# Kernel optimization log

Measured on AMD Instinct MI355X. Metric: run time of the kernel, lower is better.

The kernel has to match this reference:

```python
import jax, jax.numpy as jnp
import numpy as np

H = 150  # hidden per direction

def _lstm_dir(x, w_ih, w_hh, b_ih, b_hh):
    # x: [B, T, D] -> hs: [B, T, H]; PyTorch gate order i,f,g,o
    B = x.shape[0]
    xg = jnp.einsum('btd,gd->btg', x, w_ih) + b_ih + b_hh  # precompute input projection [B,T,4H]
    def step(carry, xt):
        h, c = carry
        g = xt + h @ w_hh.T
        i, f, gg, o = jnp.split(g, 4, axis=-1)
        i, f, o = jax.nn.sigmoid(i), jax.nn.sigmoid(f), jax.nn.sigmoid(o)
        c = f * c + i * jnp.tanh(gg)
        h = o * jnp.tanh(c)
        return (h, c), h
    init = (jnp.zeros((B, H), x.dtype), jnp.zeros((B, H), x.dtype))
    _, hs = jax.lax.scan(step, init, jnp.swapaxes(xg, 0, 1))  # [T,B,H]
    return jnp.swapaxes(hs, 0, 1)

def _bilstm(x, w_ih_f, w_hh_f, b_ih_f, b_hh_f, w_ih_b, w_hh_b, b_ih_b, b_hh_b):
    fwd = _lstm_dir(x, w_ih_f, w_hh_f, b_ih_f, b_hh_f)
    bwd = jnp.flip(_lstm_dir(jnp.flip(x, axis=1), w_ih_b, w_hh_b, b_ih_b, b_hh_b), axis=1)
    return jnp.concatenate([fwd, bwd], axis=-1)  # [B, T, 2H]

def setup_inputs() -> dict:
    key = jax.random.key(0)
    ks = jax.random.split(key, 20)
    s = 0.05
    d = {
        'sentences': jax.random.normal(ks[0], (1024, 128, 343), jnp.float32),
        'w_ih_f1': jax.random.normal(ks[1], (600, 343)) * s,
        'w_hh_f1': jax.random.normal(ks[2], (600, 150)) * s,
        'b_ih_f1': jax.random.normal(ks[3], (600,)) * s,
        'b_hh_f1': jax.random.normal(ks[4], (600,)) * s,
        'w_ih_b1': jax.random.normal(ks[5], (600, 343)) * s,
        'w_hh_b1': jax.random.normal(ks[6], (600, 150)) * s,
        'b_ih_b1': jax.random.normal(ks[7], (600,)) * s,
        'b_hh_b1': jax.random.normal(ks[8], (600,)) * s,
        'w_ih_f2': jax.random.normal(ks[9], (600, 300)) * s,
        'w_hh_f2': jax.random.normal(ks[10], (600, 150)) * s,
        'b_ih_f2': jax.random.normal(ks[11], (600,)) * s,
        'b_hh_f2': jax.random.normal(ks[12], (600,)) * s,
        'w_ih_b2': jax.random.normal(ks[13], (600, 300)) * s,
        'w_hh_b2': jax.random.normal(ks[14], (600, 150)) * s,
        'b_ih_b2': jax.random.normal(ks[15], (600,)) * s,
        'b_hh_b2': jax.random.normal(ks[16], (600,)) * s,
        'w_out': jax.random.normal(ks[17], (7, 300)) * s,
        'b_out': jax.random.normal(ks[18], (7,)) * s,
    }
    return d

def reference(sentences, w_ih_f1, w_hh_f1, b_ih_f1, b_hh_f1, w_ih_b1, w_hh_b1, b_ih_b1, b_hh_b1,
              w_ih_f2, w_hh_f2, b_ih_f2, b_hh_f2, w_ih_b2, w_hh_b2, b_ih_b2, b_hh_b2, w_out, b_out):
    # Layer 1: per-sentence BiLSTM over words, batched instead of a python loop (dropout is eval-mode identity)
    word_out = _bilstm(sentences, w_ih_f1, w_hh_f1, b_ih_f1, b_hh_f1, w_ih_b1, w_hh_b1, b_ih_b1, b_hh_b1)  # [S,T,300]
    sent_emb = jnp.max(word_out, axis=1)  # max-pool over words -> [S,300]
    # Layer 2: BiLSTM over the sequence of sentence embeddings (batch of 1 paragraph)
    sent_out = _bilstm(sent_emb[None], w_ih_f2, w_hh_f2, b_ih_f2, b_hh_f2, w_ih_b2, w_hh_b2, b_ih_b2, b_hh_b2)[0]  # [S,300]
    log_probs = jax.nn.log_softmax(sent_out @ w_out.T + b_out, axis=-1)  # [S,7]
    return log_probs
```

## Files before the change

### kernel.cpp

```cpp
#include <hip/hip_runtime.h>
#include <hip/hip_bf16.h>
#include <hip/hip_fp16.h>

typedef short bf16x8 __attribute__((ext_vector_type(8)));
typedef float f32x4 __attribute__((ext_vector_type(4)));
typedef unsigned short u16x4 __attribute__((ext_vector_type(4)));
typedef unsigned int uint32;

#define MFMA_B16(a,b,c) __builtin_amdgcn_mfma_f32_16x16x32_bf16(a,b,c,0,0,0)

#define NS   1024
#define TLEN 128
#define DD   343
#define HH   150
#define GG   600
#define KX   352
#define XR   360
#define HR   168
#define KXP  44
#define NP   640
#define NG2  640

#define OFF_WXP  0u
#define OFF_WHP  901120u
#define OFF_B1   1310720u
#define OFF_W2B  1315840u
#define OFF_W2I  1725440u
#define OFF_SE   3184640u
#define OFF_XG2  4413440u
#define OFF_H2O  9656320u
#define OFF_XBF  10885120u
#define NEED_BF  103159808ull
#define OFF_XG1  103159808ull
#define NEED_SPLIT 774248448ull

#define PE0 450560
#define PE1 655360
#define PE2 656640
#define PE3 861440
#define PE4 1226240

__device__ __forceinline__ float rcp_fast(float x) { return __builtin_amdgcn_rcpf(x); }
__device__ __forceinline__ float sigm(float x) { return rcp_fast(1.f + __expf(-x)); }
__device__ __forceinline__ float tanh_fast(float x) { return 1.f - 2.f * rcp_fast(__expf(2.f * x) + 1.f); }

typedef __attribute__((address_space(1))) const void GASV;
typedef __attribute__((address_space(3))) void LASV;
__device__ __forceinline__ void gload_lds16(const void* g, void* l) {
  __builtin_amdgcn_global_load_lds((GASV*)g, (LASV*)l, 16, 0, 0);
}

__device__ __forceinline__ void bar_lds() {
  asm volatile("s_waitcnt lgkmcnt(0)" ::: "memory");
  __builtin_amdgcn_s_barrier();
  asm volatile("" ::: "memory");
}
__device__ __forceinline__ void bar_full() {
  asm volatile("s_waitcnt vmcnt(0) lgkmcnt(0)" ::: "memory");
  __builtin_amdgcn_s_barrier();
  asm volatile("" ::: "memory");
}

__device__ __forceinline__ unsigned short f2bu(float v) {
  __hip_bfloat16 b = __float2bfloat16(v);
  return __builtin_bit_cast(unsigned short, b);
}

__global__ __launch_bounds__(256) void prep_kernel(
    const float* __restrict__ wif1, const float* __restrict__ whf1,
    const float* __restrict__ bif1, const float* __restrict__ bhf1,
    const float* __restrict__ wib1, const float* __restrict__ whb1,
    const float* __restrict__ bib1, const float* __restrict__ bhb1,
    const float* __restrict__ wif2, const float* __restrict__ wib2,
    const float* __restrict__ whf2, const float* __restrict__ whb2,
    __hip_bfloat16* __restrict__ WXp, __hip_bfloat16* __restrict__ WHp,
    float* __restrict__ B1, __hip_bfloat16* __restrict__ W2B, float* __restrict__ W2I)
{
  int i = blockIdx.x * 256 + threadIdx.x;
  if (i < PE0) {
    int d = i / 225280; int r = i - d * 225280;
    int p = r / 5120;   int r2 = r - p * 5120;
    int n2 = r2 >> 3;   int jj = r2 & 7;
    int k = p * 8 + jj;
    int g = n2 / 160, j = n2 - g * 160;
    const float* w = d ? wib1 : wif1;
    float v = (j < HH && k < DD) ? w[(g * HH + j) * DD + k] : 0.f;
    WXp[i] = __float2bfloat16(v);
  } else if (i < PE1) {
    int ii = i - PE0;
    int d = ii / 102400; int r = ii - d * 102400;
    int p = r / 5120;    int r2 = r - p * 5120;
    int n2 = r2 >> 3;    int jj = r2 & 7;
    int k = p * 8 + jj;
    int g = n2 / 160, j = n2 - g * 160;
    const float* w = d ? whb1 : whf1;
    float v = (j < HH && k < HH) ? w[(g * HH + j) * HH + k] : 0.f;
    WHp[ii] = __float2bfloat16(v);
  } else if (i < PE2) {
    int ii = i - PE1;
    int d = ii / NP; int n2 = ii - d * NP;
    int g = n2 / 160, j = n2 - g * 160;
    float v = 0.f;
    if (j < HH) {
      int n = g * HH + j;
      v = d ? (bib1[n] + bhb1[n]) : (bif1[n] + bhf1[n]);
    }
    B1[ii] = v;
  } else if (i < PE3) {
    int ii = i - PE2;
    int d = ii / 102400; int r = ii - d * 102400;
    int n2 = r / 160;    int k = r - n2 * 160;
    int g = n2 / 160, j = n2 - g * 160;
    const float* w = d ? whb2 : whf2;
    float v = (j < HH && k < HH) ? w[(g * HH + j) * HH + k] : 0.f;
    W2B[ii] = __float2bfloat16(v);
  } else if (i < PE4) {
    int ii = i - PE3;
    int d = ii / 182400; int r = ii - d * 182400;
    int k = r / 608;     int n = r - k * 608;
    const float* w = d ? wib2 : wif2;
    float v = (n < GG) ? w[n * 300 + k] : 0.f;
    W2I[ii] = v;
  }
}

__global__ __launch_bounds__(256) void xcvt_kernel(
    const float* __restrict__ x, __hip_bfloat16* __restrict__ XBF)
{
  const int total4 = NS * TLEN * (KX / 4);
  for (int idx = blockIdx.x * 256 + threadIdx.x; idx < total4; idx += gridDim.x * 256) {
    int row = idx / 88;
    int c4 = (idx - row * 88) * 4;
    const float* src = x + (size_t)row * DD + c4;
    float v0 = 0.f, v1 = 0.f, v2 = 0.f, v3 = 0.f;
    if (c4 + 3 < DD) {
      v0 = __builtin_nontemporal_load(src);
      v1 = __builtin_nontemporal_load(src + 1);
      v2 = __builtin_nontemporal_load(src + 2);
      v3 = __builtin_nontemporal_load(src + 3);
    } else {
      if (c4 < DD)     v0 = src[0];
      if (c4 + 1 < DD) v1 = src[1];
      if (c4 + 2 < DD) v2 = src[2];
    }
    u16x4 o;
    o.x = f2bu(v0); o.y = f2bu(v1); o.z = f2bu(v2); o.w = f2bu(v3);
    u16x4* dst = (u16x4*)((unsigned short*)XBF + (size_t)row * KX + c4);
    __builtin_nontemporal_store(o, dst);
  }
}

#define GA_SMEM (128u * 720u)

__global__ __launch_bounds__(512) void xg1_gemm(
    const __hip_bfloat16* __restrict__ XBF, const __hip_bfloat16* __restrict__ WXp,
    const float* __restrict__ B1, float* __restrict__ XG1)
{
  extern __shared__ char smem[];
  __hip_bfloat16* xsA = (__hip_bfloat16*)smem;

  const int bid = blockIdx.x;
  const int mt = bid / 10;
  const int ntile = bid - mt * 10;
  const int dir = ntile / 5;
  const int nb = (ntile - dir * 5) * 128;
  const int m0 = mt * 128;

  const int tid = threadIdx.x;
  const int lane = tid & 63;
  const int wv = tid >> 6;
  const int wr = wv >> 2;
  const int wc = wv & 3;
  const int arow = lane & 15;
  const int kgrp = lane >> 4;

  #pragma unroll
  for (int i = 0; i < 16; ++i) {
    int rid = wv * 16 + i;
    if (lane < 44) {
      const __hip_bfloat16* gp = XBF + (size_t)(m0 + rid) * KX + lane * 8;
      gload_lds16((const void*)gp, (void*)(smem + rid * 720));
    }
  }
  bar_full();

  const __hip_bfloat16* WXd = WXp + (size_t)dir * KXP * NP * 8;

  f32x4 acc[4][2];
  #pragma unroll
  for (int mi = 0; mi < 4; ++mi)
    #pragma unroll
    for (int ni = 0; ni < 2; ++ni) acc[mi][ni] = (f32x4){0.f, 0.f, 0.f, 0.f};

  for (int kk = 0; kk < 11; ++kk) {
    bf16x8 a[4], b[2];
    #pragma unroll
    for (int mi = 0; mi < 4; ++mi)
      a[mi] = *reinterpret_cast<const bf16x8*>(
          xsA + (wr * 64 + mi * 16 + arow) * XR + kk * 32 + kgrp * 8);
    #pragma unroll
    for (int ni = 0; ni < 2; ++ni)
      b[ni] = *reinterpret_cast<const bf16x8*>(
          WXd + ((size_t)(kk * 4 + kgrp) * NP + nb + wc * 32 + ni * 16 + arow) * 8);
    #pragma unroll
    for (int mi = 0; mi < 4; ++mi)
      #pragma unroll
      for (int ni = 0; ni < 2; ++ni)
        acc[mi][ni] = MFMA_B16(a[mi], b[ni], acc[mi][ni]);
  }

  float bias[2];
  #pragma unroll
  for (int ni = 0; ni < 2; ++ni)
    bias[ni] = B1[dir * NP + nb + wc * 32 + ni * 16 + arow];

  float* outd = XG1 + (size_t)dir * NS * TLEN * NG2;
  #pragma unroll
  for (int mi = 0; mi < 4; ++mi) {
    #pragma unroll
    for (int r = 0; r < 4; ++r) {
      int m = m0 + wr * 64 + mi * 16 + kgrp * 4 + r;
      int s = m >> 7, t = m & 127;
      float* row = outd + ((size_t)s * TLEN + t) * NG2;
      #pragma unroll
      for (int ni = 0; ni < 2; ++ni)
        row[nb + wc * 32 + ni * 16 + arow] = acc[mi][ni][r] + bias[ni];
    }
  }
}

__global__ __launch_bounds__(640) void lstm1_rec(
    const float* __restrict__ XG1, const __hip_bfloat16* __restrict__ WHp,
    float* __restrict__ SE)
{
  __shared__ __hip_bfloat16 hs[16 * HR];

  const int tid = threadIdx.x;
  const int lane = tid & 63;
  const int wv = tid >> 6;
  const int dir = blockIdx.x & 1;
  const int s0 = (blockIdx.x >> 1) * 8;
  const int c16 = lane & 15;
  const int kgrp = lane >> 4;
  const int j = wv * 16 + c16;

  for (int e = tid; e < 16 * HR; e += 640) hs[e] = __float2bfloat16(0.f);

  const __hip_bfloat16* WHd = WHp + (size_t)dir * 20 * NP * 8;
  bf16x8 whr[5][4];
  #pragma unroll
  for (int kh = 0; kh < 5; ++kh)
    #pragma unroll
    for (int g4 = 0; g4 < 4; ++g4) {
      whr[kh][g4] = *reinterpret_cast<const bf16x8*>(
          WHd + ((size_t)(kh * 4 + kgrp) * NP + g4 * 160 + j) * 8);
      asm volatile("" : "+v"(whr[kh][g4]));
    }

  float creg[4] = {0.f, 0.f, 0.f, 0.f};
  float mxr[4] = {-3e38f, -3e38f, -3e38f, -3e38f};

  const float* xgd = XG1 + (size_t)dir * NS * TLEN * NG2;
  const int sentb = s0 + (kgrp & 1) * 4;
  const int par = kgrp >> 1;

  float xq[16], xqN[16];
  #pragma unroll
  for (int g4 = 0; g4 < 4; ++g4)
    #pragma unroll
    for (int r = 0; r < 4; ++r) {
      int tl = par;
      int tt = dir ? (127 - tl) : tl;
      xq[g4 * 4 + r] = xgd[((size_t)(sentb + r) * TLEN + tt) * NG2 + g4 * 160 + j];
    }
  __syncthreads();

  for (int p = 0; p < 64; ++p) {
    f32x4 acc[4];
    #pragma unroll
    for (int g4 = 0; g4 < 4; ++g4) {
      acc[g4][0] = xq[g4 * 4 + 0]; acc[g4][1] = xq[g4 * 4 + 1];
      acc[g4][2] = xq[g4 * 4 + 2]; acc[g4][3] = xq[g4 * 4 + 3];
    }
    if (p < 63) {
      #pragma unroll
      for (int g4 = 0; g4 < 4; ++g4)
        #pragma unroll
        for (int r = 0; r < 4; ++r) {
          int tl = 2 * (p + 1) + par;
          int tt = dir ? (127 - tl) : tl;
          xqN[g4 * 4 + r] = xgd[((size_t)(sentb + r) * TLEN + tt) * NG2 + g4 * 160 + j];
        }
    }
    #pragma unroll
    for (int kh = 0; kh < 5; ++kh) {
      bf16x8 ah = *reinterpret_cast<const bf16x8*>(hs + c16 * HR + kh * 32 + kgrp * 8);
      #pragma unroll
      for (int g4 = 0; g4 < 4; ++g4)
        acc[g4] = MFMA_B16(ah, whr[kh][g4], acc[g4]);
    }
    {
      const bool act = (kgrp < 2);
      #pragma unroll
      for (int r = 0; r < 4; ++r) {
        float iv = sigm(acc[0][r]);
        float fv = sigm(acc[1][r]);
        float gv = tanh_fast(acc[2][r]);
        float ov = sigm(acc[3][r]);
        float cin = __shfl_xor(creg[r], 32);
        float cn = fv * cin + iv * gv;
        float h = ov * tanh_fast(cn);
        creg[r] = act ? cn : creg[r];
        mxr[r] = act ? fmaxf(mxr[r], h) : mxr[r];
        if (act) hs[(8 + kgrp * 4 + r) * HR + j] = __float2bfloat16(h);
      }
    }
    bar_lds();
    #pragma unroll
    for (int kh = 0; kh < 5; ++kh) {
      bf16x8 ah = *reinterpret_cast<const bf16x8*>(hs + c16 * HR + kh * 32 + kgrp * 8);
      #pragma unroll
      for (int g4 = 0; g4 < 4; ++g4)
        acc[g4] = MFMA_B16(ah, whr[kh][g4], acc[g4]);
    }
    {
      const bool act = (kgrp >= 2);
      #pragma unroll
      for (int r = 0; r < 4; ++r) {
        float iv = sigm(acc[0][r]);
        float fv = sigm(acc[1][r]);
        float gv = tanh_fast(acc[2][r]);
        float ov = sigm(acc[3][r]);
        float cin = __shfl_xor(creg[r], 32);
        float cn = fv * cin + iv * gv;
        float h = ov * tanh_fast(cn);
        creg[r] = act ? cn : creg[r];
        mxr[r] = act ? fmaxf(mxr[r], h) : mxr[r];
        if (act) {
          int s = (kgrp - 2) * 4 + r;
          hs[s * HR + j] = __float2bfloat16(h);
          hs[(8 + s) * HR + j] = __float2bfloat16(0.f);
        }
      }
    }
    bar_lds();
    #pragma unroll
    for (int q = 0; q < 16; ++q) xq[q] = xqN[q];
  }

  #pragma unroll
  for (int r = 0; r < 4; ++r) {
    float m = fmaxf(mxr[r], __shfl_xor(mxr[r], 32));
    if (kgrp < 2 && j < HH)
      SE[(size_t)(s0 + kgrp * 4 + r) * 300 + dir * HH + j] = m;
  }
}

#define XS_SZ   46080u
#define HS_OFF  (2u * XS_SZ)
#define L1_SMEM (HS_OFF + 5376u)

template<bool BF>
__device__ __forceinline__ void stage_x(char* xsd, const float* __restrict__ x,
                                        const __hip_bfloat16* __restrict__ XBF,
                                        int t0, int dir, int s0, int tid, int lane, int wv)
{
  if constexpr (BF) {
    #pragma unroll
    for (int i = 0; i < 7; ++i) {
      int rid = wv + i * 10;
      if (rid < 64 && lane < 44) {
        int p = rid >> 4, rr = rid & 15;
        int t = t0 + 2 * p + (rr >> 3);
        int s = s0 + (rr & 7);
        int tt = dir ? (127 - t) : t;
        const __hip_bfloat16* gp = XBF + ((size_t)s * TLEN + tt) * KX + lane * 8;
        gload_lds16((const void*)gp, (void*)(xsd + rid * 720));
      }
    }
  } else {
    for (int e = tid; e < 4 * 16 * XR; e += 640) {
      int row16 = e / XR;
      int col = e - row16 * XR;
      int p = row16 >> 4, rr = row16 & 15;
      int t = t0 + 2 * p + (rr >> 3);
      int s = s0 + (rr & 7);
      int tt = dir ? (127 - t) : t;
      float v = (col < DD) ? x[((size_t)s * TLEN + tt) * DD + col] : 0.f;
      ((__hip_bfloat16*)xsd)[e] = __float2bfloat16(v);
    }
  }
}

template<bool BF>
__global__ __launch_bounds__(640)
void lstm1_kernel(
    const float* __restrict__ x, const __hip_bfloat16* __restrict__ XBF,
    const __hip_bfloat16* __restrict__ WXp, const __hip_bfloat16* __restrict__ WHp,
    const float* __restrict__ B1, float* __restrict__ SE)
{
  extern __shared__ char smem[];
  char* xs0 = smem;
  char* xs1 = smem + XS_SZ;
  __hip_bfloat16* hs = (__hip_bfloat16*)(smem + HS_OFF);

  const int tid = threadIdx.x;
  const int lane = tid & 63;
  const int wv = tid >> 6;
  const int dir = blockIdx.x & 1;
  const int s0 = (blockIdx.x >> 1) * 8;
  const int c16 = lane & 15;
  const int kgrp = lane >> 4;
  const int j = wv * 16 + c16;

  for (int e = tid; e < 16 * HR; e += 640) hs[e] = __float2bfloat16(0.f);

  float bias[4];
  #pragma unroll
  for (int g4 = 0; g4 < 4; ++g4) {
    bias[g4] = B1[dir * NP + g4 * 160 + j];
    asm volatile("" : "+v"(bias[g4]));
  }

  const __hip_bfloat16* WXd = WXp + (size_t)dir * KXP * NP * 8;
  const __hip_bfloat16* WHd = WHp + (size_t)dir * 20 * NP * 8;

  bf16x8 whr[5][4];
  #pragma unroll
  for (int kh = 0; kh < 5; ++kh)
    #pragma unroll
    for (int g4 = 0; g4 < 4; ++g4) {
      whr[kh][g4] = *reinterpret_cast<const bf16x8*>(
          WHd + ((size_t)(kh * 4 + kgrp) * NP + g4 * 160 + j) * 8);
      asm volatile("" : "+v"(whr[kh][g4]));
    }

  float creg[4] = {0.f, 0.f, 0.f, 0.f};
  float mxr[4] = {-3e38f, -3e38f, -3e38f, -3e38f};

  stage_x<BF>(xs0, x, XBF, 0, dir, s0, tid, lane, wv);
  bar_full();

  for (int g = 0; g < 16; ++g) {
    char* xsc = (g & 1) ? xs1 : xs0;
    char* xsn = (g & 1) ? xs0 : xs1;
    const __hip_bfloat16* xsb = (const __hip_bfloat16*)xsc;

    f32x4 acc[4][4];
    #pragma unroll
    for (int p = 0; p < 4; ++p)
      #pragma unroll
      for (int g4 = 0; g4 < 4; ++g4) acc[p][g4] = (f32x4){0.f, 0.f, 0.f, 0.f};

    for (int kk = 0; kk < 11; ++kk) {
      bf16x8 a[4], b[4];
      #pragma unroll
      for (int p = 0; p < 4; ++p)
        a[p] = *reinterpret_cast<const bf16x8*>(xsb + (p * 16 + c16) * XR + kk * 32 + kgrp * 8);
      #pragma unroll
      for (int g4 = 0; g4 < 4; ++g4)
        b[g4] = *reinterpret_cast<const bf16x8*>(
            WXd + ((size_t)(kk * 4 + kgrp) * NP + g4 * 160 + j) * 8);
      #pragma unroll
      for (int p = 0; p < 4; ++p)
        #pragma unroll
        for (int g4 = 0; g4 < 4; ++g4)
          acc[p][g4] = MFMA_B16(a[p], b[g4], acc[p][g4]);
    }

    if (g < 15)
      stage_x<BF>(xsn, x, XBF, (g + 1) * 8, dir, s0, tid, lane, wv);

    #pragma unroll
    for (int p = 0; p < 4; ++p) {
      #pragma unroll
      for (int kh = 0; kh < 5; ++kh) {
        bf16x8 ah = *reinterpret_cast<const bf16x8*>(hs + c16 * HR + kh * 32 + kgrp * 8);
        #pragma unroll
        for (int g4 = 0; g4 < 4; ++g4)
          acc[p][g4] = MFMA_B16(ah, whr[kh][g4], acc[p][g4]);
      }
      {
        const bool act = (kgrp < 2);
        #pragma unroll
        for (int r = 0; r < 4; ++r) {
          float iv = sigm(acc[p][0][r] + bias[0]);
          float fv = sigm(acc[p][1][r] + bias[1]);
          float gv = tanh_fast(acc[p][2][r] + bias[2]);
          float ov = sigm(acc[p][3][r] + bias[3]);
          float cin = __shfl_xor(creg[r], 32);
          float cn = fv * cin + iv * gv;
          float h = ov * tanh_fast(cn);
          creg[r] = act ? cn : creg[r];
          mxr[r] = act ? fmaxf(mxr[r], h) : mxr[r];
          if (act) hs[(8 + kgrp * 4 + r) * HR + j] = __float2bfloat16(h);
        }
      }
      bar_lds();
      #pragma unroll
      for (int kh = 0; kh < 5; ++kh) {
        bf16x8 ah = *reinterpret_cast<const bf16x8*>(hs + c16 * HR + kh * 32 + kgrp * 8);
        #pragma unroll
        for (int g4 = 0; g4 < 4; ++g4)
          acc[p][g4] = MFMA_B16(ah, whr[kh][g4], acc[p][g4]);
      }
      {
        const bool act = (kgrp >= 2);
        #pragma unroll
        for (int r = 0; r < 4; ++r) {
          float iv = sigm(acc[p][0][r] + bias[0]);
          float fv = sigm(acc[p][1][r] + bias[1]);
          float gv = tanh_fast(acc[p][2][r] + bias[2]);
          float ov = sigm(acc[p][3][r] + bias[3]);
          float cin = __shfl_xor(creg[r], 32);
          float cn = fv * cin + iv * gv;
          float h = ov * tanh_fast(cn);
          creg[r] = act ? cn : creg[r];
          mxr[r] = act ? fmaxf(mxr[r], h) : mxr[r];
          if (act) {
            int s = (kgrp - 2) * 4 + r;
            hs[s * HR + j] = __float2bfloat16(h);
            hs[(8 + s) * HR + j] = __float2bfloat16(0.f);
          }
        }
      }
      if (p == 3) bar_full(); else bar_lds();
    }
  }

  #pragma unroll
  for (int r = 0; r < 4; ++r) {
    float m = fmaxf(mxr[r], __shfl_xor(mxr[r], 32));
    if (kgrp < 2 && j < HH)
      SE[(size_t)(s0 + kgrp * 4 + r) * 300 + dir * HH + j] = m;
  }
}

__global__ __launch_bounds__(256, 1) void xg2_kernel(
    const float* __restrict__ SE, const float* __restrict__ W2I,
    const float* __restrict__ bif2, const float* __restrict__ bhf2,
    const float* __restrict__ bib2, const float* __restrict__ bhb2,
    float* __restrict__ XG2)
{
  __shared__ float se[32 * 304];
  const int d = blockIdx.x >> 5, st = blockIdx.x & 31, sb = st * 32;
  const int tid = threadIdx.x;
  for (int e = tid; e < 32 * 300; e += 256) {
    int si = e / 300, k = e - si * 300;
    se[si * 304 + k] = SE[(size_t)(sb + si) * 300 + k];
  }
  __syncthreads();
  for (int pass = 0; pass < 3; ++pass) {
    int n = pass * 256 + tid;
    if (n < GG) {
      int n2 = (n / 150) * 160 + (n % 150);
      float bias = d ? (bib2[n] + bhb2[n]) : (bif2[n] + bhf2[n]);
      float acc[32];
      #pragma unroll
      for (int si = 0; si < 32; ++si) acc[si] = bias;
      const float* wcol = W2I + (size_t)d * 300 * 608 + n;
      for (int k = 0; k < 300; ++k) {
        float wvv = wcol[(size_t)k * 608];
        #pragma unroll
        for (int si = 0; si < 32; ++si) acc[si] += wvv * se[si * 304 + k];
      }
      #pragma unroll
      for (int si = 0; si < 32; ++si)
        XG2[((size_t)d * NS + sb + si) * NG2 + n2] = acc[si];
    }
  }
  for (int e = tid; e < 32 * 40; e += 256) {
    int si = e / 40, q = e - si * 40;
    int g = q / 10, jp = 150 + (q - g * 10);
    XG2[((size_t)d * NS + sb + si) * NG2 + g * 160 + jp] = 0.f;
  }
}

__global__ __launch_bounds__(640) void lstm2_kernel(
    const __hip_bfloat16* __restrict__ W2B, const float* __restrict__ XG2,
    float* __restrict__ H2O)
{
  const int dir = blockIdx.x;
  const int tid = threadIdx.x;
  const int lane = tid & 63;
  const int wv = tid >> 6;
  const int c16 = lane & 15;
  const int kg = lane >> 4;
  const int j = wv * 16 + c16;
  __shared__ __align__(16) __hip_bfloat16 hbuf[2][160];

  const f32x4 ZERO4 = {0.f, 0.f, 0.f, 0.f};

  const __hip_bfloat16* Wd = W2B + (size_t)dir * NP * 160;
  bf16x8 wf[5][4];
  #pragma unroll
  for (int kt = 0; kt < 5; ++kt)
    #pragma unroll
    for (int g4 = 0; g4 < 4; ++g4) {
      wf[kt][g4] = *reinterpret_cast<const bf16x8*>(
          Wd + (size_t)(g4 * 160 + j) * 160 + kt * 32 + kg * 8);
      asm volatile("" : "+v"(wf[kt][g4]));
    }

  if (tid < 160) hbuf[0][tid] = __float2bfloat16(0.f);
  __syncthreads();

  float creg = 0.f;
  const float* xg = XG2 + (size_t)dir * NS * NG2;

  float xqC[8], xqN[8];
  #pragma unroll
  for (int q = 0; q < 2; ++q)
    #pragma unroll
    for (int g4 = 0; g4 < 4; ++g4) {
      int sl = q;
      int ss2 = dir ? (1023 - sl) : sl;
      xqC[q * 4 + g4] = xg[(size_t)ss2 * NG2 + g4 * 160 + j];
    }

  for (int grp = 0; grp < 512; ++grp) {
    #pragma unroll
    for (int q = 0; q < 2; ++q)
      #pragma unroll
      for (int g4 = 0; g4 < 4; ++g4) {
        int sl = grp * 2 + 2 + q;
        if (sl < 1024) {
          int ss2 = dir ? (1023 - sl) : sl;
          xqN[q * 4 + g4] = xg[(size_t)ss2 * NG2 + g4 * 160 + j];
        } else {
          xqN[q * 4 + g4] = 0.f;
        }
      }
    #pragma unroll
    for (int q = 0; q < 2; ++q) {
      const int step = grp * 2 + q;
      const int ss = dir ? (1023 - step) : step;
      bf16x8 hf[5];
      #pragma unroll
      for (int kt = 0; kt < 5; ++kt)
        hf[kt] = *reinterpret_cast<const bf16x8*>(&hbuf[q][kt * 32 + kg * 8]);
      f32x4 aA[4], aB[4];
      #pragma unroll
      for (int g4 = 0; g4 < 4; ++g4) {
        aA[g4] = MFMA_B16(hf[0], wf[0][g4], ZERO4);
        aB[g4] = MFMA_B16(hf[1], wf[1][g4], ZERO4);
      }
      #pragma unroll
      for (int g4 = 0; g4 < 4; ++g4) {
        aA[g4] = MFMA_B16(hf[2], wf[2][g4], aA[g4]);
        aB[g4] = MFMA_B16(hf[3], wf[3][g4], aB[g4]);
        aA[g4] = MFMA_B16(hf[4], wf[4][g4], aA[g4]);
      }
      float iv = sigm(aA[0][0] + aB[0][0] + xqC[q * 4 + 0]);
      float fv = sigm(aA[1][0] + aB[1][0] + xqC[q * 4 + 1]);
      float gv = tanh_fast(aA[2][0] + aB[2][0] + xqC[q * 4 + 2]);
      float ov = sigm(aA[3][0] + aB[3][0] + xqC[q * 4 + 3]);
      creg = fv * creg + iv * gv;
      float nh = ov * tanh_fast(creg);
      if (kg == 0) {
        hbuf[q ^ 1][j] = __float2bfloat16(nh);
        if (j < HH) H2O[(size_t)ss * 300 + dir * HH + j] = nh;
      }
      bar_lds();
    }
    #pragma unroll
    for (int q = 0; q < 8; ++q) xqC[q] = xqN[q];
  }
}

__global__ __launch_bounds__(256, 1) void head_kernel(
    const float* __restrict__ H2O, const float* __restrict__ w_out,
    const float* __restrict__ b_out, float* __restrict__ out)
{
  int s = blockIdx.x * 256 + threadIdx.x;
  if (s >= NS) return;
  float acc[7];
  #pragma unroll
  for (int c = 0; c < 7; ++c) acc[c] = b_out[c];
  const float* hrow = H2O + (size_t)s * 300;
  for (int k = 0; k < 300; ++k) {
    float hv = hrow[k];
    #pragma unroll
    for (int c = 0; c < 7; ++c) acc[c] += hv * w_out[c * 300 + k];
  }
  float m = acc[0];
  #pragma unroll
  for (int c = 1; c < 7; ++c) m = fmaxf(m, acc[c]);
  float sum = 0.f;
  #pragma unroll
  for (int c = 0; c < 7; ++c) sum += __expf(acc[c] - m);
  float lse = m + __logf(sum);
  #pragma unroll
  for (int c = 0; c < 7; ++c) out[s * 7 + c] = acc[c] - lse;
}

extern "C" void kernel_launch(void* const* d_in, const int* in_sizes, int n_in,
                              void* d_out, int out_size, void* d_ws, size_t ws_size,
                              hipStream_t stream) {
  const float* x      = (const float*)d_in[0];
  const float* wif1   = (const float*)d_in[1];
  const float* whf1   = (const float*)d_in[2];
  const float* bif1   = (const float*)d_in[3];
  const float* bhf1   = (const float*)d_in[4];
  const float* wib1   = (const float*)d_in[5];
  const float* whb1   = (const float*)d_in[6];
  const float* bib1   = (const float*)d_in[7];
  const float* bhb1   = (const float*)d_in[8];
  const float* wif2   = (const float*)d_in[9];
  const float* whf2   = (const float*)d_in[10];
  const float* bif2   = (const float*)d_in[11];
  const float* bhf2   = (const float*)d_in[12];
  const float* wib2   = (const float*)d_in[13];
  const float* whb2   = (const float*)d_in[14];
  const float* bib2   = (const float*)d_in[15];
  const float* bhb2   = (const float*)d_in[16];
  const float* w_out  = (const float*)d_in[17];
  const float* b_out  = (const float*)d_in[18];

  char* ws = (char*)d_ws;
  __hip_bfloat16* WXp = (__hip_bfloat16*)(ws + OFF_WXP);
  __hip_bfloat16* WHp = (__hip_bfloat16*)(ws + OFF_WHP);
  float*    B1  = (float*)(ws + OFF_B1);
  __hip_bfloat16* W2B = (__hip_bfloat16*)(ws + OFF_W2B);
  float*    W2I = (float*)(ws + OFF_W2I);
  float*    SE  = (float*)(ws + OFF_SE);
  float*    XG2 = (float*)(ws + OFF_XG2);
  float*    H2O = (float*)(ws + OFF_H2O);
  __hip_bfloat16* XBF = (__hip_bfloat16*)(ws + OFF_XBF);
  float*    XG1 = (float*)(ws + OFF_XG1);

  const bool useBF = (ws_size >= NEED_BF);
  const bool useSPLIT = (ws_size >= NEED_SPLIT);

  prep_kernel<<<(PE4 + 255) / 256, 256, 0, stream>>>(
      wif1, whf1, bif1, bhf1, wib1, whb1, bib1, bhb1,
      wif2, wib2, whf2, whb2, WXp, WHp, B1, W2B, W2I);

  if (useBF)
    xcvt_kernel<<<4096, 256, 0, stream>>>(x, XBF);

  if (useSPLIT) {
    (void)hipFuncSetAttribute((const void*)xg1_gemm,
                              hipFuncAttributeMaxDynamicSharedMemorySize, GA_SMEM);
    xg1_gemm<<<10240, 512, GA_SMEM, stream>>>(XBF, WXp, B1, XG1);
    lstm1_rec<<<256, 640, 0, stream>>>(XG1, WHp, SE);
  } else {
    (void)hipFuncSetAttribute((const void*)(lstm1_kernel<true>),
                              hipFuncAttributeMaxDynamicSharedMemorySize, L1_SMEM);
    (void)hipFuncSetAttribute((const void*)(lstm1_kernel<false>),
                              hipFuncAttributeMaxDynamicSharedMemorySize, L1_SMEM);
    if (useBF)
      lstm1_kernel<true><<<256, 640, L1_SMEM, stream>>>(x, XBF, WXp, WHp, B1, SE);
    else
      lstm1_kernel<false><<<256, 640, L1_SMEM, stream>>>(x, XBF, WXp, WHp, B1, SE);
  }

  xg2_kernel<<<64, 256, 0, stream>>>(SE, W2I, bif2, bhf2, bib2, bhb2, XG2);

  lstm2_kernel<<<2, 640, 0, stream>>>(W2B, XG2, H2O);

  head_kernel<<<4, 256, 0, stream>>>(H2O, w_out, b_out, (float*)d_out);
}
```

Before: 1.610 ms.

## Store layer-1 input projections as bf16 and process sentences in chunks

```diff
diff --git a/kernel.cpp b/kernel.cpp
--- a/kernel.cpp
+++ b/kernel.cpp
@@ -32,7 +32,6 @@
 #define OFF_XBF  10885120u
 #define NEED_BF  103159808ull
 #define OFF_XG1  103159808ull
-#define NEED_SPLIT 774248448ull
 
 #define PE0 450560
 #define PE1 655360
@@ -154,84 +153,85 @@
 
 __global__ __launch_bounds__(512) void xg1_gemm(
     const __hip_bfloat16* __restrict__ XBF, const __hip_bfloat16* __restrict__ WXp,
-    const float* __restrict__ B1, float* __restrict__ XG1)
+    const float* __restrict__ B1, __hip_bfloat16* __restrict__ XG1,
+    int sBase, int CS)
 {
   extern __shared__ char smem[];
   __hip_bfloat16* xsA = (__hip_bfloat16*)smem;
 
   const int bid = blockIdx.x;
-  const int mt = bid / 10;
-  const int ntile = bid - mt * 10;
-  const int dir = ntile / 5;
-  const int nb = (ntile - dir * 5) * 128;
-  const int m0 = mt * 128;
+  const int dir = bid & 1;
+  const int mtl = bid >> 1;
+  const int sg = sBase + mtl;
 
   const int tid = threadIdx.x;
   const int lane = tid & 63;
   const int wv = tid >> 6;
   const int wr = wv >> 2;
   const int wc = wv & 3;
-  const int arow = lane & 15;
+  const int c16 = lane & 15;
   const int kgrp = lane >> 4;
 
   #pragma unroll
   for (int i = 0; i < 16; ++i) {
     int rid = wv * 16 + i;
     if (lane < 44) {
-      const __hip_bfloat16* gp = XBF + (size_t)(m0 + rid) * KX + lane * 8;
+      const __hip_bfloat16* gp = XBF + ((size_t)sg * TLEN + rid) * KX + lane * 8;
       gload_lds16((const void*)gp, (void*)(smem + rid * 720));
     }
   }
   bar_full();
 
   const __hip_bfloat16* WXd = WXp + (size_t)dir * KXP * NP * 8;
-
-  f32x4 acc[4][2];
-  #pragma unroll
-  for (int mi = 0; mi < 4; ++mi)
-    #pragma unroll
-    for (int ni = 0; ni < 2; ++ni) acc[mi][ni] = (f32x4){0.f, 0.f, 0.f, 0.f};
-
-  for (int kk = 0; kk < 11; ++kk) {
-    bf16x8 a[4], b[2];
+  __hip_bfloat16* outd = XG1 + ((size_t)dir * CS + mtl) * TLEN * NG2;
+
+  #pragma unroll
+  for (int nh = 0; nh < 2; ++nh) {
+    const int nbase = nh * 320 + wc * 80;
+    f32x4 acc[4][5];
     #pragma unroll
     for (int mi = 0; mi < 4; ++mi)
-      a[mi] = *reinterpret_cast<const bf16x8*>(
-          xsA + (wr * 64 + mi * 16 + arow) * XR + kk * 32 + kgrp * 8);
-    #pragma unroll
-    for (int ni = 0; ni < 2; ++ni)
-      b[ni] = *reinterpret_cast<const bf16x8*>(
-          WXd + ((size_t)(kk * 4 + kgrp) * NP + nb + wc * 32 + ni * 16 + arow) * 8);
+      #pragma unroll
+      for (int nf = 0; nf < 5; ++nf) acc[mi][nf] = (f32x4){0.f, 0.f, 0.f, 0.f};
+
+    for (int kk = 0; kk < 11; ++kk) {
+      bf16x8 a[4], b[5];
+      #pragma unroll
+      for (int mi = 0; mi < 4; ++mi)
+        a[mi] = *reinterpret_cast<const bf16x8*>(
+            xsA + (wr * 64 + mi * 16 + c16) * XR + kk * 32 + kgrp * 8);
+      #pragma unroll
+      for (int nf = 0; nf < 5; ++nf)
+        b[nf] = *reinterpret_cast<const bf16x8*>(
+            WXd + ((size_t)(kk * 4 + kgrp) * NP + nbase + nf * 16 + c16) * 8);
+      #pragma unroll
+      for (int mi = 0; mi < 4; ++mi)
+        #pragma unroll
+        for (int nf = 0; nf < 5; ++nf)
+          acc[mi][nf] = MFMA_B16(a[mi], b[nf], acc[mi][nf]);
+    }
+
+    float bias[5];
+    #pragma unroll
+    for (int nf = 0; nf < 5; ++nf)
+      bias[nf] = B1[dir * NP + nbase + nf * 16 + c16];
+
     #pragma unroll
     for (int mi = 0; mi < 4; ++mi)
       #pragma unroll
-      for (int ni = 0; ni < 2; ++ni)
-        acc[mi][ni] = MFMA_B16(a[mi], b[ni], acc[mi][ni]);
-  }
-
-  float bias[2];
-  #pragma unroll
-  for (int ni = 0; ni < 2; ++ni)
-    bias[ni] = B1[dir * NP + nb + wc * 32 + ni * 16 + arow];
-
-  float* outd = XG1 + (size_t)dir * NS * TLEN * NG2;
-  #pragma unroll
-  for (int mi = 0; mi < 4; ++mi) {
-    #pragma unroll
-    for (int r = 0; r < 4; ++r) {
-      int m = m0 + wr * 64 + mi * 16 + kgrp * 4 + r;
-      int s = m >> 7, t = m & 127;
-      float* row = outd + ((size_t)s * TLEN + t) * NG2;
-      #pragma unroll
-      for (int ni = 0; ni < 2; ++ni)
-        row[nb + wc * 32 + ni * 16 + arow] = acc[mi][ni][r] + bias[ni];
-    }
+      for (int r = 0; r < 4; ++r) {
+        int t = wr * 64 + mi * 16 + kgrp * 4 + r;
+        __hip_bfloat16* row = outd + (size_t)t * NG2;
+        #pragma unroll
+        for (int nf = 0; nf < 5; ++nf)
+          row[nbase + nf * 16 + c16] = __float2bfloat16(acc[mi][nf][r] + bias[nf]);
+      }
   }
 }
 
 __global__ __launch_bounds__(640) void lstm1_rec(
-    const float* __restrict__ XG1, const __hip_bfloat16* __restrict__ WHp,
-    float* __restrict__ SE)
+    const __hip_bfloat16* __restrict__ XG1, const __hip_bfloat16* __restrict__ WHp,
+    float* __restrict__ SE, int sBase, int CS)
 {
   __shared__ __hip_bfloat16 hs[16 * HR];
 
@@ -239,7 +239,9 @@
   const int lane = tid & 63;
   const int wv = tid >> 6;
   const int dir = blockIdx.x & 1;
-  const int s0 = (blockIdx.x >> 1) * 8;
+  const int grp = blockIdx.x >> 1;
+  const int cls0 = grp * 8;
+  const int s0g = sBase + cls0;
   const int c16 = lane & 15;
   const int kgrp = lane >> 4;
   const int j = wv * 16 + c16;
@@ -260,8 +262,8 @@
   float creg[4] = {0.f, 0.f, 0.f, 0.f};
   float mxr[4] = {-3e38f, -3e38f, -3e38f, -3e38f};
 
-  const float* xgd = XG1 + (size_t)dir * NS * TLEN * NG2;
-  const int sentb = s0 + (kgrp & 1) * 4;
+  const __hip_bfloat16* xgd = XG1 + (size_t)dir * CS * TLEN * NG2;
+  const int sentb = cls0 + (kgrp & 1) * 4;
   const int par = kgrp >> 1;
 
   float xq[16], xqN[16];
@@ -269,9 +271,9 @@
   for (int g4 = 0; g4 < 4; ++g4)
     #pragma unroll
     for (int r = 0; r < 4; ++r) {
-      int tl = par;
-      int tt = dir ? (127 - tl) : tl;
-      xq[g4 * 4 + r] = xgd[((size_t)(sentb + r) * TLEN + tt) * NG2 + g4 * 160 + j];
+      int tt = dir ? (127 - par) : par;
+      xq[g4 * 4 + r] = __bfloat162float(
+          xgd[((size_t)(sentb + r) * TLEN + tt) * NG2 + g4 * 160 + j]);
     }
   __syncthreads();
 
@@ -289,7 +291,8 @@
         for (int r = 0; r < 4; ++r) {
           int tl = 2 * (p + 1) + par;
           int tt = dir ? (127 - tl) : tl;
-          xqN[g4 * 4 + r] = xgd[((size_t)(sentb + r) * TLEN + tt) * NG2 + g4 * 160 + j];
+          xqN[g4 * 4 + r] = __bfloat162float(
+              xgd[((size_t)(sentb + r) * TLEN + tt) * NG2 + g4 * 160 + j]);
         }
     }
     #pragma unroll
@@ -352,7 +355,7 @@
   for (int r = 0; r < 4; ++r) {
     float m = fmaxf(mxr[r], __shfl_xor(mxr[r], 32));
     if (kgrp < 2 && j < HH)
-      SE[(size_t)(s0 + kgrp * 4 + r) * 300 + dir * HH + j] = m;
+      SE[(size_t)(s0g + kgrp * 4 + r) * 300 + dir * HH + j] = m;
   }
 }
 
@@ -613,8 +616,7 @@
   for (int q = 0; q < 2; ++q)
     #pragma unroll
     for (int g4 = 0; g4 < 4; ++g4) {
-      int sl = q;
-      int ss2 = dir ? (1023 - sl) : sl;
+      int ss2 = dir ? (1023 - q) : q;
       xqC[q * 4 + g4] = xg[(size_t)ss2 * NG2 + g4 * 160 + j];
     }
 
@@ -727,10 +729,16 @@
   float*    XG2 = (float*)(ws + OFF_XG2);
   float*    H2O = (float*)(ws + OFF_H2O);
   __hip_bfloat16* XBF = (__hip_bfloat16*)(ws + OFF_XBF);
-  float*    XG1 = (float*)(ws + OFF_XG1);
+  __hip_bfloat16* XG1 = (__hip_bfloat16*)(ws + OFF_XG1);
 
   const bool useBF = (ws_size >= NEED_BF);
-  const bool useSPLIT = (ws_size >= NEED_SPLIT);
+
+  int CS = 0;
+  if (useBF && ws_size >= NEED_BF + 128ull * 327680ull) {
+    size_t avail = ws_size - NEED_BF;
+    CS = 1024;
+    while ((size_t)CS * 327680ull > avail) CS >>= 1;
+  }
 
   prep_kernel<<<(PE4 + 255) / 256, 256, 0, stream>>>(
       wif1, whf1, bif1, bhf1, wib1, whb1, bib1, bhb1,
@@ -739,11 +747,13 @@
   if (useBF)
     xcvt_kernel<<<4096, 256, 0, stream>>>(x, XBF);
 
-  if (useSPLIT) {
+  if (CS > 0) {
     (void)hipFuncSetAttribute((const void*)xg1_gemm,
                               hipFuncAttributeMaxDynamicSharedMemorySize, GA_SMEM);
-    xg1_gemm<<<10240, 512, GA_SMEM, stream>>>(XBF, WXp, B1, XG1);
-    lstm1_rec<<<256, 640, 0, stream>>>(XG1, WHp, SE);
+    for (int sBase = 0; sBase < NS; sBase += CS) {
+      xg1_gemm<<<2 * CS, 512, GA_SMEM, stream>>>(XBF, WXp, B1, XG1, sBase, CS);
+      lstm1_rec<<<CS / 4, 640, 0, stream>>>(XG1, WHp, SE, sBase, CS);
+    }
   } else {
     (void)hipFuncSetAttribute((const void*)(lstm1_kernel<true>),
                               hipFuncAttributeMaxDynamicSharedMemorySize, L1_SMEM);
```

New measurement: 1.376 ms. 14.5% less time.
